# Optimization experiments

Hardware: AMD Instinct MI355X
Metric: run time of the kernel (lower is better)

The kernel has to match this reference:

```python
import jax, jax.numpy as jnp
import numpy as np

V, D, H, L, RATIO, T_MAX = 1024, 512, 8, 11, 3, 1024
DH = D // H
HID = D * RATIO
NB, DB = 2048, 128  # bigram buckets / dim
EPS = 1e-6


def _rope_tables(T):
    pos = jnp.arange(T, dtype=jnp.float32)
    freqs = 1.0 / (10000.0 ** (jnp.arange(0, DH, 2, dtype=jnp.float32) / DH))
    emb = jnp.outer(pos, freqs)  # [T, DH/2]
    return jnp.cos(emb), jnp.sin(emb)


def _rmsnorm(x, w):
    return x * jax.lax.rsqrt(jnp.mean(x * x, axis=-1, keepdims=True) + EPS) * w


def setup_inputs() -> dict:
    key = jax.random.key(0)
    ks = jax.random.split(key, 10)
    B, T = 8, 1024
    s = 0.02
    return {
        "x": jax.random.randint(ks[0], (B, T), 0, V),
        "embed": jax.random.normal(ks[1], (V, D), jnp.float32) * s,
        "Wqkv": jax.random.normal(ks[2], (L, 3 * D, D), jnp.float32) * s,
        "Wproj": jax.random.normal(ks[3], (L, D, D), jnp.float32) * s,
        "n1_w": jnp.ones((L, D), jnp.float32),
        "n2_w": jnp.ones((L, D), jnp.float32),
        "Wfc1": jax.random.normal(ks[4], (L, HID, D), jnp.float32) * s,
        "Wfc2": jax.random.normal(ks[5], (L, D, HID), jnp.float32) * s,
        "norm_f_w": jnp.ones((D,), jnp.float32),
        "bg_embed": jax.random.normal(ks[6], (NB, DB), jnp.float32) * s,
        "bg_proj": jax.random.normal(ks[7], (V, DB), jnp.float32) * s,
    }


def _attn(x, Wqkv, Wproj, cos, sin, causal):
    B, T, C = x.shape
    qkv = x @ Wqkv.T  # [B,T,3D]
    q, k, v = jnp.split(qkv, 3, axis=-1)
    def heads(t):
        return t.reshape(B, T, H, DH).transpose(0, 2, 1, 3)  # [B,H,T,DH]
    q, k, v = heads(q), heads(k), heads(v)
    c = cos[None, None]  # [1,1,T,DH/2]
    s = sin[None, None]
    def rope(t):
        t1, t2 = t[..., : DH // 2], t[..., DH // 2 :]
        return jnp.concatenate([t1 * c - t2 * s, t1 * s + t2 * c], axis=-1)
    q, k = rope(q), rope(k)
    w = jnp.einsum("bhqd,bhkd->bhqk", q, k) * (DH ** -0.5)
    w = jnp.where(causal, w, -jnp.inf)
    w = jax.nn.softmax(w.astype(jnp.float32), axis=-1).astype(x.dtype)
    out = jnp.einsum("bhqk,bhkd->bhqd", w, v)
    self_w = jnp.diagonal(w, axis1=-2, axis2=-1)[..., None]  # [B,H,T,1]
    out = out - self_w * v  # XSA: subtract self-value contribution
    out = out.transpose(0, 2, 1, 3).reshape(B, T, C)
    return out @ Wproj.T


def reference(x, embed, Wqkv, Wproj, n1_w, n2_w, Wfc1, Wfc2, norm_f_w, bg_embed, bg_proj):
    B, T = x.shape
    cos, sin = _rope_tables(T_MAX)
    cos, sin = cos[:T], sin[:T]
    causal = jnp.tril(jnp.ones((T, T), dtype=bool))
    # bigram logits from previous token
    prev = jnp.concatenate([jnp.zeros((B, 1), x.dtype), x[:, :-1]], axis=1)
    bigram_logits = bg_embed[prev % NB] @ bg_proj.T  # [B,T,V]
    h = embed[x]
    for i in range(L):
        h = h + _attn(_rmsnorm(h, n1_w[i]), Wqkv[i], Wproj[i], cos, sin, causal)
        z = _rmsnorm(h, n2_w[i])
        h = h + jnp.square(jax.nn.relu(z @ Wfc1[i].T)) @ Wfc2[i].T
    h = _rmsnorm(h, norm_f_w)
    return h @ embed.T + bigram_logits
```

## Files before the change

### kernel.cpp

```cpp
#include <hip/hip_runtime.h>

#define NROW   8192
#define DMODEL 512
#define TSEQ   1024
#define LAYERS 11
#define HIDDEN 1536

typedef __bf16 bf16_t;
typedef bf16_t bf16x8 __attribute__((ext_vector_type(8)));
typedef bf16_t bf16x4 __attribute__((ext_vector_type(4)));
typedef float  f32x4  __attribute__((ext_vector_type(4)));
typedef unsigned int u32;
typedef u32 u32x4 __attribute__((ext_vector_type(4)));

#define GLD16(gp, lp) __builtin_amdgcn_global_load_lds( \
    (const __attribute__((address_space(1))) void*)(gp), \
    (__attribute__((address_space(3))) void*)(lp), 16, 0, 0)

__global__ void rope_table_k(float* __restrict__ cosT, float* __restrict__ sinT) {
    int i = blockIdx.x * blockDim.x + threadIdx.x;
    int t = i >> 5, j = i & 31;
    float freq = powf(10000.f, -(float)j * (1.f / 32.f));
    float ang = (float)t * freq;
    cosT[i] = cosf(ang);
    sinT[i] = sinf(ang);
}

__global__ void embed_gather_k(const int* __restrict__ x,
                               const float* __restrict__ embed,
                               float* __restrict__ h) {
    int n = blockIdx.x;
    int d = threadIdx.x;
    const float4* e = (const float4*)(embed + (size_t)x[n] * DMODEL);
    float4* hp = (float4*)(h + (size_t)n * DMODEL);
    hp[d] = e[d];
}

__global__ void bg_gather_k(const int* __restrict__ x,
                            const float* __restrict__ bge,
                            bf16_t* __restrict__ Afu) {
    int n = blockIdx.x;
    int t = n & (TSEQ - 1);
    int prev = (t == 0) ? 0 : x[n - 1];
    Afu[(size_t)n * 640 + 512 + threadIdx.x] = (bf16_t)bge[(size_t)prev * 128 + threadIdx.x];
}

__global__ void cvt_bf16_k(const float* __restrict__ in, bf16_t* __restrict__ out, int n8) {
    int i = blockIdx.x * blockDim.x + threadIdx.x;
    if (i >= n8) return;
    float4 a = ((const float4*)in)[2 * i];
    float4 b = ((const float4*)in)[2 * i + 1];
    bf16x8 o;
    o[0] = (bf16_t)a.x; o[1] = (bf16_t)a.y; o[2] = (bf16_t)a.z; o[3] = (bf16_t)a.w;
    o[4] = (bf16_t)b.x; o[5] = (bf16_t)b.y; o[6] = (bf16_t)b.z; o[7] = (bf16_t)b.w;
    ((bf16x8*)out)[i] = o;
}

__global__ void cvt_pad_k(const float* __restrict__ in, bf16_t* __restrict__ out,
                          int n8, int lshift, int mask, int colOff) {
    int i = blockIdx.x * blockDim.x + threadIdx.x;
    if (i >= n8) return;
    int i8 = i * 8;
    int row = i8 >> lshift;
    int col = i8 & mask;
    float4 a = ((const float4*)in)[2 * i];
    float4 b = ((const float4*)in)[2 * i + 1];
    bf16x8 o;
    o[0] = (bf16_t)a.x; o[1] = (bf16_t)a.y; o[2] = (bf16_t)a.z; o[3] = (bf16_t)a.w;
    o[4] = (bf16_t)b.x; o[5] = (bf16_t)b.y; o[6] = (bf16_t)b.z; o[7] = (bf16_t)b.w;
    *(bf16x8*)&out[(size_t)row * 640 + colOff + col] = o;
}

__global__ __launch_bounds__(256) void rmsnorm_k(const float* __restrict__ in,
                                                 const float* __restrict__ w,
                                                 bf16_t* __restrict__ out,
                                                 int ostride) {
    int wv = threadIdx.x >> 6, lane = threadIdx.x & 63;
    int row = (blockIdx.x << 2) + wv;
    const float* rp = in + (size_t)row * DMODEL + lane * 8;
    float4 v0 = *(const float4*)(rp);
    float4 v1 = *(const float4*)(rp + 4);
    float ss = v0.x*v0.x + v0.y*v0.y + v0.z*v0.z + v0.w*v0.w
             + v1.x*v1.x + v1.y*v1.y + v1.z*v1.z + v1.w*v1.w;
#pragma unroll
    for (int off = 32; off; off >>= 1) ss += __shfl_xor(ss, off, 64);
    float sc = rsqrtf(ss * (1.f / DMODEL) + 1e-6f);
    const float* wp = w + lane * 8;
    float4 w0 = *(const float4*)(wp);
    float4 w1 = *(const float4*)(wp + 4);
    bf16x8 o;
    o[0] = (bf16_t)(v0.x * sc * w0.x); o[1] = (bf16_t)(v0.y * sc * w0.y);
    o[2] = (bf16_t)(v0.z * sc * w0.z); o[3] = (bf16_t)(v0.w * sc * w0.w);
    o[4] = (bf16_t)(v1.x * sc * w1.x); o[5] = (bf16_t)(v1.y * sc * w1.y);
    o[6] = (bf16_t)(v1.z * sc * w1.z); o[7] = (bf16_t)(v1.w * sc * w1.w);
    *(bf16x8*)(out + (size_t)row * ostride + lane * 8) = o;
}

template<int BM, int EPI>
__global__ __launch_bounds__(256) void gemm_mfma(const bf16_t* __restrict__ A,
                                                 const bf16_t* __restrict__ B,
                                                 float* __restrict__ Cf,
                                                 bf16_t* __restrict__ Cb,
                                                 const float* __restrict__ cosT,
                                                 const float* __restrict__ sinT,
                                                 int M, int N, int K, int nbx) {
    constexpr int MI  = BM / 32;
    constexpr int ACH = BM / 64;
    __shared__ __align__(16) bf16_t As[3][BM * 32];
    __shared__ __align__(16) bf16_t Bs[3][128 * 32];
    const int tid = threadIdx.x;
    const int w = tid >> 6, lane = tid & 63;

    const int nwg = (int)gridDim.x;
    const int bid = blockIdx.x;
    const int swz = (bid & 7) * (nwg >> 3) + (bid >> 3);
    const int bx = swz % nbx, by = swz / nbx;

    const int m0 = by * BM, n0 = bx * 128;
    const int wr = (w >> 1) * (BM / 2), wc = (w & 1) * 64;
    const int fr = lane & 15, fq = lane >> 4;

    f32x4 acc[MI][4] = {};

    auto stage = [&](int k0, int buf) {
#pragma unroll
        for (int c = 0; c < ACH; ++c) {
            int idx = c * 256 + tid;
            int row = idx >> 2, cs = idx & 3;
            GLD16(A + (size_t)(m0 + row) * K + k0 + cs * 8,
                  &As[buf][(size_t)(c * 256 + w * 64) * 8]);
        }
#pragma unroll
        for (int c = 0; c < 2; ++c) {
            int idx = c * 256 + tid;
            int row = idx >> 2, cs = idx & 3;
            GLD16(B + (size_t)(n0 + row) * K + k0 + cs * 8,
                  &Bs[buf][(size_t)(c * 256 + w * 64) * 8]);
        }
    };

    const int NK = K >> 5;
    stage(0, 0);
    stage(32, 1);
    for (int k = 0; k < NK; ++k) {
        const int cur = k % 3;
        if (k + 2 < NK) {
            stage((k + 2) << 5, (k + 2) % 3);
            if constexpr (BM == 128) asm volatile("s_waitcnt vmcnt(8)" ::: "memory");
            else                     asm volatile("s_waitcnt vmcnt(6)" ::: "memory");
        } else if (k + 1 < NK) {
            if constexpr (BM == 128) asm volatile("s_waitcnt vmcnt(4)" ::: "memory");
            else                     asm volatile("s_waitcnt vmcnt(3)" ::: "memory");
        } else {
            asm volatile("s_waitcnt vmcnt(0)" ::: "memory");
        }
        __builtin_amdgcn_s_barrier();
        __builtin_amdgcn_sched_barrier(0);

        bf16x8 a[MI], b[4];
        const bf16_t* ap = &As[cur][(size_t)(wr + fr) * 32 + fq * 8];
        const bf16_t* bp = &Bs[cur][(size_t)(wc + fr) * 32 + fq * 8];
#pragma unroll
        for (int i = 0; i < MI; ++i) a[i] = *(const bf16x8*)(ap + i * 16 * 32);
#pragma unroll
        for (int j = 0; j < 4; ++j)  b[j] = *(const bf16x8*)(bp + j * 16 * 32);
#pragma unroll
        for (int i = 0; i < MI; ++i)
#pragma unroll
            for (int j = 0; j < 4; ++j)
                acc[i][j] = __builtin_amdgcn_mfma_f32_16x16x32_bf16(a[i], b[j], acc[i][j], 0, 0, 0);

        asm volatile("s_waitcnt lgkmcnt(0)" ::: "memory");
        __builtin_amdgcn_s_barrier();
        __builtin_amdgcn_sched_barrier(0);
    }

    if (EPI == 4) {
        const bool qk = (n0 + wc) < 1024;
#pragma unroll
        for (int i = 0; i < MI; ++i) {
#pragma unroll
            for (int q = 0; q < 4; ++q) {
                int row = m0 + wr + i * 16 + fq * 4 + q;
                size_t rb = (size_t)row * N + n0 + wc;
                if (qk) {
                    int t = row & (TSEQ - 1);
#pragma unroll
                    for (int j = 0; j < 2; ++j) {
                        int d = j * 16 + fr;
                        float c = cosT[t * 32 + d];
                        float s = sinT[t * 32 + d];
                        float v1 = acc[i][j][q], v2 = acc[i][j + 2][q];
                        Cb[rb + j * 16 + fr]       = (bf16_t)(v1 * c - v2 * s);
                        Cb[rb + (j + 2) * 16 + fr] = (bf16_t)(v1 * s + v2 * c);
                    }
                } else {
#pragma unroll
                    for (int j = 0; j < 4; ++j)
                        Cb[rb + j * 16 + fr] = (bf16_t)acc[i][j][q];
                }
            }
        }
        return;
    }
#pragma unroll
    for (int i = 0; i < MI; ++i) {
        int row = m0 + wr + i * 16 + fq * 4;
#pragma unroll
        for (int j = 0; j < 4; ++j) {
            int col = n0 + wc + j * 16 + fr;
#pragma unroll
            for (int q = 0; q < 4; ++q) {
                float v = acc[i][j][q];
                size_t off = (size_t)(row + q) * N + col;
                if (EPI == 0)      Cf[off] = v;
                else if (EPI == 1) Cf[off] += v;
                else if (EPI == 2) { v = fmaxf(v, 0.f); Cb[off] = (bf16_t)(v * v); }
            }
        }
    }
}

__global__ __launch_bounds__(256) void attn_mfma_k(const bf16_t* __restrict__ qkvb,
                                                   bf16_t* __restrict__ outb) {
    __shared__ __align__(16) bf16_t Ks[2][64 * 64];
    __shared__ __align__(16) bf16_t VsT[2][2 * 64 * 32];

    const int tid = threadIdx.x;
    const int w  = tid >> 6;
    const int ln = tid & 63;
    const int lr = ln & 15;
    const int lg = ln >> 4;

    const int bid = blockIdx.x;
    const int qb = 15 - (bid >> 6);
    const int bh = bid & 63;
    const int b = bh >> 3, h = bh & 7;
    const int tq0b = qb << 6;
    const int tq0  = tq0b + w * 16;
    const int qrow = tq0 + lr;

    const bf16_t* Qg = qkvb + (size_t)b * TSEQ * 1536 + h * 64;
    const bf16_t* Kg = Qg + 512;
    const bf16_t* Vg = Qg + 1024;

    const int mk = tid >> 4;
    const int md = tid & 15;
    const int src0 = lr + 32 * (lg & 1);
    const int fsel = lg >> 1;
    const int gofs = 8 * (lg ^ ((lr >> 2) & 3));

    auto KSTAGE = [&](int t0, int buf) {
#pragma unroll
        for (int ii = 0; ii < 2; ++ii) {
            const int i = w * 2 + ii;
            int key = i * 8 + (ln >> 3);
            int dc  = (ln & 7) ^ (ln >> 3);
            GLD16(Kg + (size_t)(t0 + key) * 1536 + dc * 8, &Ks[buf][i * 512]);
        }
    };
    auto VLOAD = [&](int t0, bf16x4* rv) {
#pragma unroll
        for (int i = 0; i < 4; ++i)
            rv[i] = *(const bf16x4*)(Vg + (size_t)(t0 + mk * 4 + i) * 1536 + md * 4);
    };
    auto VWRITE = [&](const bf16x4* rv, int buf) {
        const int s = mk >> 3;
#pragma unroll
        for (int j = 0; j < 4; ++j) {
            int row = md * 4 + j;
            bf16x4 wv;
            wv[0] = rv[0][j]; wv[1] = rv[1][j]; wv[2] = rv[2][j]; wv[3] = rv[3][j];
            int g = (mk & 7) ^ ((md & 3) << 1);
            *(bf16x4*)&VsT[buf][s * 2048 + row * 32 + g * 4] = wv;
        }
    };

    bf16x8 qreg[2];
    {
        const bf16_t* qp = Qg + (size_t)qrow * 1536 + lg * 8;
        qreg[0] = *(const bf16x8*)qp;
        qreg[1] = *(const bf16x8*)(qp + 32);
#pragma unroll
        for (int j = 0; j < 8; ++j) {
            qreg[0][j] = (bf16_t)((float)qreg[0][j] * 0.125f);
            qreg[1][j] = (bf16_t)((float)qreg[1][j] * 0.125f);
        }
    }

    f32x4 accO[4] = {};
    float mrun = -1e30f, pl = 0.f, esf = 0.f;

    {
        bf16x4 rv[4];
        KSTAGE(0, 0);
        VLOAD(0, rv);
        asm volatile("s_waitcnt vmcnt(0)" ::: "memory");
        VWRITE(rv, 0);
        asm volatile("s_waitcnt lgkmcnt(0)" ::: "memory");
        __builtin_amdgcn_s_barrier();
        __builtin_amdgcn_sched_barrier(0);
    }

    for (int t0 = 0; t0 <= tq0b; t0 += 64) {
        const int cur = (t0 >> 6) & 1;
        const bool more = t0 < tq0b;
        bf16x4 rv[4];
        if (more) {
            KSTAGE(t0 + 64, cur ^ 1);
            VLOAD(t0 + 64, rv);
        }

        f32x4 sq[4] = {};
#pragma unroll
        for (int kr = 0; kr < 4; ++kr) {
            int key = kr * 16 + lr;
#pragma unroll
            for (int s = 0; s < 2; ++s) {
                int chunk = key * 8 + ((s * 4 + lg) ^ (key & 7));
                bf16x8 kf = *(const bf16x8*)&Ks[cur][chunk * 8];
                sq[kr] = __builtin_amdgcn_mfma_f32_16x16x32_bf16(kf, qreg[s], sq[kr], 0, 0, 0);
            }
        }

        float pv[4][4];
        float tm = -1e30f;
#pragma unroll
        for (int f = 0; f < 4; ++f)
#pragma unroll
            for (int r = 0; r < 4; ++r) {
                int key = t0 + f * 16 + lg * 4 + r;
                float sv = (key <= qrow) ? sq[f][r] : -1e30f;
                pv[f][r] = sv;
                tm = fmaxf(tm, sv);
            }
        tm = fmaxf(tm, __shfl_xor(tm, 16, 64));
        tm = fmaxf(tm, __shfl_xor(tm, 32, 64));

        const bool resc = __any(tm > mrun + 8.f);
        float mnew = resc ? fmaxf(mrun, tm) : mrun;
        float psum = 0.f, pd = 0.f;
        float e16[4][4];
#pragma unroll
        for (int f = 0; f < 4; ++f)
#pragma unroll
            for (int r = 0; r < 4; ++r) {
                float e = __expf(pv[f][r] - mnew);
                e16[f][r] = e;
                psum += e;
                int key = t0 + f * 16 + lg * 4 + r;
                pd = (key == qrow) ? e : pd;
            }
        if (resc) {
            float corr = __expf(mrun - mnew);
            mrun = mnew;
            pl  = pl  * corr + psum;
            esf = esf * corr + pd;
#pragma unroll
            for (int dblk = 0; dblk < 4; ++dblk)
#pragma unroll
                for (int r = 0; r < 4; ++r) accO[dblk][r] *= corr;
        } else {
            pl  += psum;
            esf += pd;
        }

        u32 plo[4], phi[4];
#pragma unroll
        for (int f = 0; f < 4; ++f) {
            bf16x4 t;
            t[0] = (bf16_t)e16[f][0]; t[1] = (bf16_t)e16[f][1];
            t[2] = (bf16_t)e16[f][2]; t[3] = (bf16_t)e16[f][3];
            uint2 pr = __builtin_bit_cast(uint2, t);
            plo[f] = pr.x; phi[f] = pr.y;
        }

#pragma unroll
        for (int s = 0; s < 2; ++s) {
            u32 a0 = (u32)__shfl((int)plo[s * 2],     src0,      64);
            u32 a1 = (u32)__shfl((int)phi[s * 2],     src0,      64);
            u32 a2 = (u32)__shfl((int)plo[s * 2],     src0 + 16, 64);
            u32 a3 = (u32)__shfl((int)phi[s * 2],     src0 + 16, 64);
            u32 c0 = (u32)__shfl((int)plo[s * 2 + 1], src0,      64);
            u32 c1 = (u32)__shfl((int)phi[s * 2 + 1], src0,      64);
            u32 c2 = (u32)__shfl((int)plo[s * 2 + 1], src0 + 16, 64);
            u32 c3 = (u32)__shfl((int)phi[s * 2 + 1], src0 + 16, 64);
            u32x4 bw;
            bw[0] = fsel ? c0 : a0;
            bw[1] = fsel ? c1 : a1;
            bw[2] = fsel ? c2 : a2;
            bw[3] = fsel ? c3 : a3;
            bf16x8 bfrag = __builtin_bit_cast(bf16x8, bw);
#pragma unroll
            for (int dblk = 0; dblk < 4; ++dblk) {
                bf16x8 av = *(const bf16x8*)&VsT[cur][s * 2048 + (dblk * 16 + lr) * 32 + gofs];
                accO[dblk] = __builtin_amdgcn_mfma_f32_16x16x32_bf16(av, bfrag, accO[dblk], 0, 0, 0);
            }
        }

        if (more) {
            asm volatile("s_waitcnt vmcnt(0)" ::: "memory");
            VWRITE(rv, cur ^ 1);
            asm volatile("s_waitcnt lgkmcnt(0)" ::: "memory");
            __builtin_amdgcn_s_barrier();
            __builtin_amdgcn_sched_barrier(0);
        }
    }

    pl  += __shfl_xor(pl, 16, 64);  pl  += __shfl_xor(pl, 32, 64);
    esf += __shfl_xor(esf, 16, 64); esf += __shfl_xor(esf, 32, 64);
    float rin = 1.0f / pl;
    const bf16_t* vqp = Vg + (size_t)qrow * 1536;
    bf16_t* op = outb + (size_t)(b * TSEQ + qrow) * DMODEL + h * 64;
#pragma unroll
    for (int dblk = 0; dblk < 4; ++dblk) {
        bf16x4 vq = *(const bf16x4*)(vqp + dblk * 16 + lg * 4);
        bf16x4 o4;
#pragma unroll
        for (int r = 0; r < 4; ++r)
            o4[r] = (bf16_t)((accO[dblk][r] - esf * (float)vq[r]) * rin);
        *(bf16x4*)(op + dblk * 16 + lg * 4) = o4;
    }
}

static inline void cvt(const float* in, bf16_t* out, size_t n, hipStream_t s) {
    int n8 = (int)(n / 8);
    cvt_bf16_k<<<(n8 + 255) / 256, 256, 0, s>>>(in, out, n8);
}

extern "C" void kernel_launch(void* const* d_in, const int* in_sizes, int n_in,
                              void* d_out, int out_size, void* d_ws, size_t ws_size,
                              hipStream_t stream) {
    const int*   x     = (const int*)d_in[0];
    const float* embed = (const float*)d_in[1];
    const float* Wqkv  = (const float*)d_in[2];
    const float* Wproj = (const float*)d_in[3];
    const float* n1w   = (const float*)d_in[4];
    const float* n2w   = (const float*)d_in[5];
    const float* Wfc1  = (const float*)d_in[6];
    const float* Wfc2  = (const float*)d_in[7];
    const float* normf = (const float*)d_in[8];
    const float* bge   = (const float*)d_in[9];
    const float* bgp   = (const float*)d_in[10];
    float* out = (float*)d_out;

    float* ws   = (float*)d_ws;
    float* cosT = ws;
    float* sinT = cosT + 32768;
    float* h    = sinT + 32768;
    bf16_t* qkvb = (bf16_t*)(h + (size_t)NROW * DMODEL);
    bf16_t* ub   = qkvb;
    bf16_t* Afu  = qkvb;
    bf16_t* xn   = qkvb + (size_t)NROW * 1536;
    bf16_t* atb  = xn  + (size_t)NROW * DMODEL;
    bf16_t* wqb  = atb + (size_t)NROW * DMODEL;
    bf16_t* wpb  = wqb + (size_t)LAYERS * 3 * DMODEL * DMODEL;
    bf16_t* w1b  = wpb + (size_t)LAYERS * DMODEL * DMODEL;
    bf16_t* w2b  = w1b + (size_t)LAYERS * HIDDEN * DMODEL;
    bf16_t* bfu  = w2b + (size_t)LAYERS * DMODEL * HIDDEN;

    rope_table_k<<<128, 256, 0, stream>>>(cosT, sinT);
    embed_gather_k<<<NROW, 128, 0, stream>>>(x, embed, h);

    cvt(Wqkv,  wqb,  (size_t)LAYERS * 3 * DMODEL * DMODEL, stream);
    cvt(Wproj, wpb,  (size_t)LAYERS * DMODEL * DMODEL, stream);
    cvt(Wfc1,  w1b,  (size_t)LAYERS * HIDDEN * DMODEL, stream);
    cvt(Wfc2,  w2b,  (size_t)LAYERS * DMODEL * HIDDEN, stream);
    cvt_pad_k<<<(65536 + 255) / 256, 256, 0, stream>>>(embed, bfu, 65536, 9, 511, 0);
    cvt_pad_k<<<(16384 + 255) / 256, 256, 0, stream>>>(bgp,   bfu, 16384, 7, 127, 512);

    for (int i = 0; i < LAYERS; ++i) {
        rmsnorm_k<<<NROW / 4, 256, 0, stream>>>(h, n1w + i * DMODEL, xn, DMODEL);
        gemm_mfma<128, 4><<<768, 256, 0, stream>>>(
            xn, wqb + (size_t)i * 3 * DMODEL * DMODEL, nullptr, qkvb,
            cosT, sinT, NROW, 3 * DMODEL, DMODEL, 12);
        attn_mfma_k<<<1024, 256, 0, stream>>>(qkvb, atb);
        gemm_mfma<64, 1><<<512, 256, 0, stream>>>(
            atb, wpb + (size_t)i * DMODEL * DMODEL, h, nullptr,
            nullptr, nullptr, NROW, DMODEL, DMODEL, 4);
        rmsnorm_k<<<NROW / 4, 256, 0, stream>>>(h, n2w + i * DMODEL, xn, DMODEL);
        gemm_mfma<128, 2><<<768, 256, 0, stream>>>(
            xn, w1b + (size_t)i * HIDDEN * DMODEL, nullptr, ub,
            nullptr, nullptr, NROW, HIDDEN, DMODEL, 12);
        gemm_mfma<64, 1><<<512, 256, 0, stream>>>(
            ub, w2b + (size_t)i * DMODEL * HIDDEN, h, nullptr,
            nullptr, nullptr, NROW, DMODEL, HIDDEN, 4);
    }

    rmsnorm_k<<<NROW / 4, 256, 0, stream>>>(h, normf, Afu, 640);
    bg_gather_k<<<NROW, 128, 0, stream>>>(x, bge, Afu);
    gemm_mfma<64, 0><<<1024, 256, 0, stream>>>(
        Afu, bfu, out, nullptr, nullptr, nullptr, NROW, 1024, 640, 8);
}
```

Before: 1.592 ms.

## Use 256-row GEMM tiles for QKV/FC1 and streamline attention softmax

The QKV and FC1 GEMMs now use a 256x128 tile run by 512 threads (8 waves), which halves the grid and raises reuse of each B tile. The shared staging loops are generalised to the new thread count. Separately, the attention softmax folds log2(e) into the Q pre-scale and uses exp2. Causal masking and the self-weight extraction now run only on the diagonal key tile. The risk is the larger tile: the launch-bounds hint of 4 blocks per CU can squeeze the register budget, and the LDS footprint is bigger, which may cause spills or lower occupancy.

```diff
diff --git a/kernel.cpp b/kernel.cpp
--- a/kernel.cpp
+++ b/kernel.cpp
@@ -16,6 +16,12 @@
 #define GLD16(gp, lp) __builtin_amdgcn_global_load_lds( \
     (const __attribute__((address_space(1))) void*)(gp), \
     (__attribute__((address_space(3))) void*)(lp), 16, 0, 0)
+
+#if __has_builtin(__builtin_amdgcn_exp2f)
+#define EXP2(x) __builtin_amdgcn_exp2f(x)
+#else
+#define EXP2(x) exp2f(x)
+#endif
 
 __global__ void rope_table_k(float* __restrict__ cosT, float* __restrict__ sinT) {
     int i = blockIdx.x * blockDim.x + threadIdx.x;
@@ -97,15 +103,19 @@
 }
 
 template<int BM, int EPI>
-__global__ __launch_bounds__(256) void gemm_mfma(const bf16_t* __restrict__ A,
-                                                 const bf16_t* __restrict__ B,
-                                                 float* __restrict__ Cf,
-                                                 bf16_t* __restrict__ Cb,
-                                                 const float* __restrict__ cosT,
-                                                 const float* __restrict__ sinT,
-                                                 int M, int N, int K, int nbx) {
-    constexpr int MI  = BM / 32;
-    constexpr int ACH = BM / 64;
+__global__ __launch_bounds__(BM == 256 ? 512 : 256, BM == 256 ? 4 : 2)
+void gemm_mfma(const bf16_t* __restrict__ A,
+               const bf16_t* __restrict__ B,
+               float* __restrict__ Cf,
+               bf16_t* __restrict__ Cb,
+               const float* __restrict__ cosT,
+               const float* __restrict__ sinT,
+               int M, int N, int K, int nbx) {
+    constexpr int NT  = (BM == 256) ? 512 : 256;
+    constexpr int WM  = (BM == 256) ? 4 : 2;
+    constexpr int MI  = BM / WM / 16;
+    constexpr int ACH = (BM * 4) / NT;
+    constexpr int BCH = 512 / NT;
     __shared__ __align__(16) bf16_t As[3][BM * 32];
     __shared__ __align__(16) bf16_t Bs[3][128 * 32];
     const int tid = threadIdx.x;
@@ -117,7 +127,7 @@
     const int bx = swz % nbx, by = swz / nbx;
 
     const int m0 = by * BM, n0 = bx * 128;
-    const int wr = (w >> 1) * (BM / 2), wc = (w & 1) * 64;
+    const int wr = (w >> 1) * (BM / WM), wc = (w & 1) * 64;
     const int fr = lane & 15, fq = lane >> 4;
 
     f32x4 acc[MI][4] = {};
@@ -125,17 +135,17 @@
     auto stage = [&](int k0, int buf) {
 #pragma unroll
         for (int c = 0; c < ACH; ++c) {
-            int idx = c * 256 + tid;
+            int idx = c * NT + tid;
             int row = idx >> 2, cs = idx & 3;
             GLD16(A + (size_t)(m0 + row) * K + k0 + cs * 8,
-                  &As[buf][(size_t)(c * 256 + w * 64) * 8]);
-        }
-#pragma unroll
-        for (int c = 0; c < 2; ++c) {
-            int idx = c * 256 + tid;
+                  &As[buf][(size_t)(c * NT + w * 64) * 8]);
+        }
+#pragma unroll
+        for (int c = 0; c < BCH; ++c) {
+            int idx = c * NT + tid;
             int row = idx >> 2, cs = idx & 3;
             GLD16(B + (size_t)(n0 + row) * K + k0 + cs * 8,
-                  &Bs[buf][(size_t)(c * 256 + w * 64) * 8]);
+                  &Bs[buf][(size_t)(c * NT + w * 64) * 8]);
         }
     };
 
@@ -278,13 +288,14 @@
 
     bf16x8 qreg[2];
     {
+        const float QS = 0.1803368801f;
         const bf16_t* qp = Qg + (size_t)qrow * 1536 + lg * 8;
         qreg[0] = *(const bf16x8*)qp;
         qreg[1] = *(const bf16x8*)(qp + 32);
 #pragma unroll
         for (int j = 0; j < 8; ++j) {
-            qreg[0][j] = (bf16_t)((float)qreg[0][j] * 0.125f);
-            qreg[1][j] = (bf16_t)((float)qreg[1][j] * 0.125f);
+            qreg[0][j] = (bf16_t)((float)qreg[0][j] * QS);
+            qreg[1][j] = (bf16_t)((float)qreg[1][j] * QS);
         }
     }
 
@@ -305,6 +316,7 @@
     for (int t0 = 0; t0 <= tq0b; t0 += 64) {
         const int cur = (t0 >> 6) & 1;
         const bool more = t0 < tq0b;
+        const bool masked = t0 == tq0b;
         bf16x4 rv[4];
         if (more) {
             KSTAGE(t0 + 64, cur ^ 1);
@@ -323,36 +335,53 @@
             }
         }
 
-        float pv[4][4];
+        float e16[4][4];
         float tm = -1e30f;
-#pragma unroll
-        for (int f = 0; f < 4; ++f)
-#pragma unroll
-            for (int r = 0; r < 4; ++r) {
-                int key = t0 + f * 16 + lg * 4 + r;
-                float sv = (key <= qrow) ? sq[f][r] : -1e30f;
-                pv[f][r] = sv;
-                tm = fmaxf(tm, sv);
-            }
+        if (masked) {
+#pragma unroll
+            for (int f = 0; f < 4; ++f)
+#pragma unroll
+                for (int r = 0; r < 4; ++r) {
+                    int key = t0 + f * 16 + lg * 4 + r;
+                    float sv = (key <= qrow) ? sq[f][r] : -1e30f;
+                    e16[f][r] = sv;
+                    tm = fmaxf(tm, sv);
+                }
+        } else {
+#pragma unroll
+            for (int f = 0; f < 4; ++f)
+#pragma unroll
+                for (int r = 0; r < 4; ++r) {
+                    e16[f][r] = sq[f][r];
+                    tm = fmaxf(tm, sq[f][r]);
+                }
+        }
         tm = fmaxf(tm, __shfl_xor(tm, 16, 64));
         tm = fmaxf(tm, __shfl_xor(tm, 32, 64));
 
         const bool resc = __any(tm > mrun + 8.f);
         float mnew = resc ? fmaxf(mrun, tm) : mrun;
-        float psum = 0.f, pd = 0.f;
-        float e16[4][4];
+        float psum = 0.f;
 #pragma unroll
         for (int f = 0; f < 4; ++f)
 #pragma unroll
             for (int r = 0; r < 4; ++r) {
-                float e = __expf(pv[f][r] - mnew);
+                float e = EXP2(e16[f][r] - mnew);
                 e16[f][r] = e;
                 psum += e;
-                int key = t0 + f * 16 + lg * 4 + r;
-                pd = (key == qrow) ? e : pd;
             }
+        float pd = 0.f;
+        if (masked) {
+#pragma unroll
+            for (int f = 0; f < 4; ++f)
+#pragma unroll
+                for (int r = 0; r < 4; ++r) {
+                    int key = t0 + f * 16 + lg * 4 + r;
+                    pd = (key == qrow) ? e16[f][r] : pd;
+                }
+        }
         if (resc) {
-            float corr = __expf(mrun - mnew);
+            float corr = EXP2(mrun - mnew);
             mrun = mnew;
             pl  = pl  * corr + psum;
             esf = esf * corr + pd;
@@ -471,7 +500,7 @@
 
     for (int i = 0; i < LAYERS; ++i) {
         rmsnorm_k<<<NROW / 4, 256, 0, stream>>>(h, n1w + i * DMODEL, xn, DMODEL);
-        gemm_mfma<128, 4><<<768, 256, 0, stream>>>(
+        gemm_mfma<256, 4><<<384, 512, 0, stream>>>(
             xn, wqb + (size_t)i * 3 * DMODEL * DMODEL, nullptr, qkvb,
             cosT, sinT, NROW, 3 * DMODEL, DMODEL, 12);
         attn_mfma_k<<<1024, 256, 0, stream>>>(qkvb, atb);
@@ -479,7 +508,7 @@
             atb, wpb + (size_t)i * DMODEL * DMODEL, h, nullptr,
             nullptr, nullptr, NROW, DMODEL, DMODEL, 4);
         rmsnorm_k<<<NROW / 4, 256, 0, stream>>>(h, n2w + i * DMODEL, xn, DMODEL);
-        gemm_mfma<128, 2><<<768, 256, 0, stream>>>(
+        gemm_mfma<256, 2><<<384, 512, 0, stream>>>(
             xn, w1b + (size_t)i * HIDDEN * DMODEL, nullptr, ub,
             nullptr, nullptr, NROW, HIDDEN, DMODEL, 12);
         gemm_mfma<64, 1><<<512, 256, 0, stream>>>(
```

Result: no change. 1.603 ms (+0.6%).
